# Performance work log

Measured on AMD Instinct MI355X. Metric: run time of the kernel, lower is better.

Reference implementation:

```python
import jax, jax.numpy as jnp
import numpy as np

N_NODES = 50000
N_EDGES = 800000
F_IN = 128
F_OUT = 128
EPS_STD = 1e-5  # PyG StdAggregation epsilon


def setup_inputs() -> dict:
    key = jax.random.key(0)
    ks = jax.random.split(key, 8)
    x = jax.random.normal(ks[0], (N_NODES, F_IN), dtype=jnp.float32)
    edge_index = jax.random.randint(ks[1], (2, N_EDGES), 0, N_NODES, dtype=jnp.int64)
    s = 0.02
    # pre_nn: Linear(2*F_IN -> F_IN)
    W_pre = jax.random.normal(ks[2], (2 * F_IN, F_IN), dtype=jnp.float32) * s
    b_pre = jnp.zeros((F_IN,), dtype=jnp.float32)
    # post_nn: Linear((1 + 4 aggregators * 1 scaler) * F_IN -> F_OUT)
    W_post = jax.random.normal(ks[3], (5 * F_IN, F_OUT), dtype=jnp.float32) * s
    b_post = jnp.zeros((F_OUT,), dtype=jnp.float32)
    # final lin: Linear(F_OUT -> F_OUT)
    W_lin = jax.random.normal(ks[4], (F_OUT, F_OUT), dtype=jnp.float32) * s
    b_lin = jnp.zeros((F_OUT,), dtype=jnp.float32)
    return {"x": x, "W_pre": W_pre, "b_pre": b_pre, "W_post": W_post,
            "b_post": b_post, "W_lin": W_lin, "b_lin": b_lin,
            "edge_index": edge_index}


def _pna_forward(x, W_pre, b_pre, W_post, b_post, W_lin, b_lin, edge_index):
    N = x.shape[0]
    src = edge_index[0]  # x_j (source / neighbor)
    dst = edge_index[1]  # x_i (target / aggregation index)

    # per-edge message: Linear(cat(x_i, x_j))  [E, F_IN]
    h = jnp.concatenate([x[dst], x[src]], axis=-1) @ W_pre + b_pre

    ones = jnp.ones((h.shape[0],), dtype=h.dtype)
    deg = jax.ops.segment_sum(ones, dst, num_segments=N)          # in-degree [N]
    deg_c = jnp.maximum(deg, 1.0)[:, None]

    s1 = jax.ops.segment_sum(h, dst, num_segments=N)
    s2 = jax.ops.segment_sum(h * h, dst, num_segments=N)
    mean = s1 / deg_c
    var = jax.nn.relu(s2 / deg_c - mean * mean)
    std = jnp.sqrt(var + EPS_STD)

    has_nb = (deg > 0)[:, None]
    mx = jax.ops.segment_max(h, dst, num_segments=N)
    mn = jax.ops.segment_min(h, dst, num_segments=N)
    mx = jnp.where(has_nb, mx, 0.0)
    mn = jnp.where(has_nb, mn, 0.0)

    # aggregators in declared order: mean, max, min, std -> [N, 4*F_IN]
    agg = jnp.concatenate([mean, mx, mn, std], axis=-1)

    # 'linear' degree scaler: deg / avg_deg
    avg_deg = jnp.mean(deg)
    agg = agg * (deg[:, None] / avg_deg)

    out = jnp.concatenate([x, agg], axis=-1) @ W_post + b_post
    out = out @ W_lin + b_lin
    return jax.nn.relu(out)


def reference(x, W_pre, b_pre, W_post, b_post, W_lin, b_lin, edge_index):
    return _pna_forward(x, W_pre, b_pre, W_post, b_post, W_lin, b_lin, edge_index)
```

## Files before the change

### kernel.cpp

```cpp
#include <hip/hip_runtime.h>
#include <hip/hip_bf16.h>
#include <math.h>


typedef _Float16 f16;
typedef _Float16 f16x8 __attribute__((ext_vector_type(8)));
typedef _Float16 f16x2 __attribute__((ext_vector_type(2)));
typedef float    f32x4 __attribute__((ext_vector_type(4)));

__device__ __forceinline__ unsigned packh2(float a, float b) {
  union { unsigned u; f16x2 h; } x; x.h = (f16x2){(f16)a, (f16)b}; return x.u;
}
__device__ __forceinline__ float2 unpackh2(unsigned v) {
  union { unsigned u; f16x2 h; } x; x.u = v;
  return make_float2((float)x.h.x, (float)x.h.y);
}

template<int KTOT, int KO1, bool HASB, bool RELU, bool OUTF16>
__global__ __launch_bounds__(256) void gemm_reg_k(
    const f16* __restrict__ A1, const f16* __restrict__ A2,
    const f16* __restrict__ Wt, const float* __restrict__ bias,
    float* __restrict__ outF, f16* __restrict__ outH, int M, int ldOut)
{
  const int tid = threadIdx.x;
  const int l   = tid & 63;
  const int w   = tid >> 6;
  const int wr  = (w >> 1) * 32;
  const int wc  = (w & 1) * 64;
  const int li  = l & 15, kg = l >> 4;
  const int rowBase = blockIdx.x * 64;
  const int colBase = blockIdx.y * 128;
  constexpr int ld2 = (KTOT > KO1) ? (KTOT - KO1) : 1;

  int aOff[2], a2Off[2], bOff[4];
#pragma unroll
  for (int r = 0; r < 2; ++r) {
    int gr = rowBase + wr + r * 16 + li; if (gr > M - 1) gr = M - 1;
    aOff[r] = gr * KO1; a2Off[r] = gr * ld2;
  }
#pragma unroll
  for (int c = 0; c < 4; ++c) bOff[c] = (colBase + wc + c * 16 + li) * KTOT;

  f32x4 acc[2][4];
#pragma unroll
  for (int r = 0; r < 2; ++r)
#pragma unroll
    for (int c = 0; c < 4; ++c) acc[r][c] = (f32x4){0.f, 0.f, 0.f, 0.f};

  f16x8 aA[2], bA[4], aB[2], bB[4];
  auto lf = [&](int k0, f16x8 a[2], f16x8 b[4]) {
    int k = k0 + kg * 8;
    if (KO1 == KTOT || k0 < KO1) {
#pragma unroll
      for (int r = 0; r < 2; ++r) a[r] = *reinterpret_cast<const f16x8*>(A1 + aOff[r] + k);
    } else {
#pragma unroll
      for (int r = 0; r < 2; ++r) a[r] = *reinterpret_cast<const f16x8*>(A2 + a2Off[r] + (k - KO1));
    }
#pragma unroll
    for (int c = 0; c < 4; ++c) b[c] = *reinterpret_cast<const f16x8*>(Wt + bOff[c] + k);
  };

  lf(0, aA, bA);
  for (int k0 = 0; k0 < KTOT; k0 += 64) {
    lf(k0 + 32, aB, bB);
#pragma unroll
    for (int r = 0; r < 2; ++r)
#pragma unroll
      for (int c = 0; c < 4; ++c)
        acc[r][c] = __builtin_amdgcn_mfma_f32_16x16x32_f16(aA[r], bA[c], acc[r][c], 0, 0, 0);
    if (k0 + 64 < KTOT) lf(k0 + 64, aA, bA);
#pragma unroll
    for (int r = 0; r < 2; ++r)
#pragma unroll
      for (int c = 0; c < 4; ++c)
        acc[r][c] = __builtin_amdgcn_mfma_f32_16x16x32_f16(aB[r], bB[c], acc[r][c], 0, 0, 0);
  }

  float bv[4];
#pragma unroll
  for (int c = 0; c < 4; ++c) {
    int col = colBase + wc + c * 16 + li;
    bv[c] = (HASB && col < 128) ? bias[col] : 0.f;
  }

  if constexpr (OUTF16) {
    __shared__ __align__(16) f16 Ls[64][136];
#pragma unroll
    for (int c = 0; c < 4; ++c) {
      int col = wc + c * 16 + li;
#pragma unroll
      for (int r = 0; r < 2; ++r)
#pragma unroll
        for (int j = 0; j < 4; ++j) {
          float v = acc[r][c][j] + bv[c];
          if (RELU) v = fmaxf(v, 0.f);
          Ls[wr + r * 16 + kg * 4 + j][col] = (f16)v;
        }
    }
    __syncthreads();
#pragma unroll
    for (int i = 0; i < 4; ++i) {
      int s = tid + 256 * i;
      int rr = s >> 4, cc = (s & 15) * 8;
      int gr = rowBase + rr;
      if (gr < M)
        *reinterpret_cast<float4*>(&outH[(size_t)gr * ldOut + colBase + cc]) =
            *reinterpret_cast<const float4*>(&Ls[rr][cc]);
    }
  } else {
    __shared__ __align__(16) float Lf[64][132];
#pragma unroll
    for (int c = 0; c < 4; ++c) {
      int col = wc + c * 16 + li;
#pragma unroll
      for (int r = 0; r < 2; ++r)
#pragma unroll
        for (int j = 0; j < 4; ++j) {
          float v = acc[r][c][j] + bv[c];
          if (RELU) v = fmaxf(v, 0.f);
          Lf[wr + r * 16 + kg * 4 + j][col] = v;
        }
    }
    __syncthreads();
#pragma unroll
    for (int i = 0; i < 8; ++i) {
      int s = tid + 256 * i;
      int rr = s >> 5, cc = (s & 31) * 4;
      int gr = rowBase + rr;
      if (gr < M)
        *reinterpret_cast<float4*>(&outF[(size_t)gr * ldOut + colBase + cc]) =
            *reinterpret_cast<const float4*>(&Lf[rr][cc]);
    }
  }
}

__global__ void cvt_x_k(const float* __restrict__ x, f16* __restrict__ xf, int n) {
  int i = (blockIdx.x * 256 + threadIdx.x) * 4;
  if (i < n) {
    float4 v = *reinterpret_cast<const float4*>(&x[i]);
    xf[i] = (f16)v.x; xf[i + 1] = (f16)v.y; xf[i + 2] = (f16)v.z; xf[i + 3] = (f16)v.w;
  }
}

__global__ void prep_wpre_k(const float* __restrict__ W, f16* __restrict__ Wt) {
  int e = blockIdx.x * 256 + threadIdx.x;
  if (e < 256 * 128) {
    int n = e >> 7, k = e & 127;
    float v = (n < 128) ? W[(size_t)k * 128 + n] : W[(size_t)(128 + k) * 128 + (n - 128)];
    Wt[e] = (f16)v;
  }
}

__global__ void fold_w_k(const float* __restrict__ Wpost, const float* __restrict__ bpost,
                         const float* __restrict__ Wlin,  const float* __restrict__ blin,
                         f16* __restrict__ WtComb, float* __restrict__ bcomb) {
  int e = blockIdx.x * 256 + threadIdx.x;
  if (e < 640 * 128) {
    int n = e / 640, k = e - n * 640;
    float s = 0.f;
#pragma unroll 4
    for (int m = 0; m < 128; ++m) s += Wpost[(size_t)k * 128 + m] * Wlin[(size_t)m * 128 + n];
    WtComb[(size_t)n * 640 + k] = (f16)s;
  } else if (e < 640 * 128 + 128) {
    int n = e - 640 * 128;
    float s = blin[n];
#pragma unroll 4
    for (int m = 0; m < 128; ++m) s += bpost[m] * Wlin[(size_t)m * 128 + n];
    bcomb[n] = s;
  }
}

__global__ void zero_k(int* __restrict__ p, int n) {
  int i = blockIdx.x * 256 + threadIdx.x;
  if (i < n) p[i] = 0;
}

__global__ void count_k(const int* __restrict__ ei, int* __restrict__ deg, int E) {
  int e = blockIdx.x * 256 + threadIdx.x;
  if (e < E) atomicAdd(&deg[ei[E + e]], 1);
}

__device__ __forceinline__ int blockExclScan(int v, int* wtot) {
  int lane = threadIdx.x & 63, wid = threadIdx.x >> 6;
  int x = v;
#pragma unroll
  for (int d = 1; d < 64; d <<= 1) {
    int y = __shfl_up(x, d);
    if (lane >= d) x += y;
  }
  if (lane == 63) wtot[wid] = x;
  __syncthreads();
  if (threadIdx.x == 0) {
    int s = 0;
#pragma unroll
    for (int k = 0; k < 4; ++k) { int t = wtot[k]; wtot[k] = s; s += t; }
  }
  __syncthreads();
  return wtot[wid] + x - v;
}

__global__ __launch_bounds__(256) void scan1_k(const int* __restrict__ deg,
                                               int* __restrict__ offs,
                                               int* __restrict__ partials, int n) {
  __shared__ int wtot[4];
  int i = blockIdx.x * 256 + threadIdx.x;
  int v = (i < n) ? deg[i] : 0;
  int e = blockExclScan(v, wtot);
  if (i < n) offs[i] = e;
  if (threadIdx.x == 255) partials[blockIdx.x] = e + v;
}

__global__ __launch_bounds__(256) void scan2_k(int* __restrict__ partials, int nb) {
  __shared__ int wtot[4];
  int v = (threadIdx.x < nb) ? partials[threadIdx.x] : 0;
  int e = blockExclScan(v, wtot);
  if (threadIdx.x < nb) partials[threadIdx.x] = e;
}

__global__ void scan3_k(const int* __restrict__ partials, int* __restrict__ offs,
                        int* __restrict__ cur, int n, int E) {
  int i = blockIdx.x * 256 + threadIdx.x;
  if (i < n) {
    int v = offs[i] + partials[i >> 8];
    offs[i] = v; cur[i] = v;
  }
  if (i == 0) offs[n] = E;
}

__global__ void scatter_k(const int* __restrict__ ei, int* __restrict__ cursor,
                          int* __restrict__ ssrc, int E) {
  int e = blockIdx.x * 256 + threadIdx.x;
  if (e < E) {
    int d = ei[E + e];
    int pos = atomicAdd(&cursor[d], 1);
    ssrc[pos] = ei[e];
  }
}

__global__ __launch_bounds__(256) void agg_k(
    const f16* __restrict__ CP, const int* __restrict__ offs,
    const int* __restrict__ ssrc, f16* __restrict__ AGG, int N)
{
  int w = threadIdx.x >> 6;
  int t = threadIdx.x & 63;
  int i = blockIdx.x * 4 + w;
  if (i >= N) return;
  int start = offs[i], end = offs[i + 1];
  int deg = end - start;
  unsigned* AGGu = (unsigned*)AGG;
  size_t o = (size_t)i * 256 + t;
  if (deg == 0) {
    AGGu[o] = 0u; AGGu[o + 64] = 0u; AGGu[o + 128] = 0u; AGGu[o + 192] = 0u;
    return;
  }
  const unsigned* CPu = (const unsigned*)CP;
  float s0 = 0.f, s1 = 0.f, q0 = 0.f, q1 = 0.f;
  float mx0 = -INFINITY, mx1 = -INFINITY, mn0 = INFINITY, mn1 = INFINITY;

  auto accum = [&](unsigned u) {
    float2 v = unpackh2(u);
    s0 += v.x; s1 += v.y;
    q0 = fmaf(v.x, v.x, q0); q1 = fmaf(v.y, v.y, q1);
    mx0 = fmaxf(mx0, v.x); mx1 = fmaxf(mx1, v.y);
    mn0 = fminf(mn0, v.x); mn1 = fminf(mn1, v.y);
  };

  for (int base = start; base < end; base += 64) {
    int cnt = min(end - base, 64);
    int myoff = 0;
    if (base + t < end) myoff = ssrc[base + t] * 128 + 64;
    int j = 0;
    for (; j + 4 <= cnt; j += 4) {
      int o0 = __shfl(myoff, j);
      int o1 = __shfl(myoff, j + 1);
      int o2 = __shfl(myoff, j + 2);
      int o3 = __shfl(myoff, j + 3);
      unsigned u0 = CPu[o0 + t];
      unsigned u1 = CPu[o1 + t];
      unsigned u2 = CPu[o2 + t];
      unsigned u3 = CPu[o3 + t];
      accum(u0); accum(u1); accum(u2); accum(u3);
    }
    for (; j < cnt; ++j) {
      int o0 = __shfl(myoff, j);
      accum(CPu[o0 + t]);
    }
  }

  float2 c = unpackh2(CPu[(size_t)i * 128 + t]);
  float degf = (float)deg;
  float inv = 1.f / degf;
  float m10 = s0 * inv, m11 = s1 * inv;
  float var0 = fmaxf(q0 * inv - m10 * m10, 0.f);
  float var1 = fmaxf(q1 * inv - m11 * m11, 0.f);
  float sd0 = sqrtf(var0 + 1e-5f), sd1 = sqrtf(var1 + 1e-5f);
  float sc = degf * (1.0f / 16.0f);
  AGGu[o]       = packh2((c.x + m10) * sc, (c.y + m11) * sc);
  AGGu[o + 64]  = packh2((c.x + mx0) * sc, (c.y + mx1) * sc);
  AGGu[o + 128] = packh2((c.x + mn0) * sc, (c.y + mn1) * sc);
  AGGu[o + 192] = packh2(sd0 * sc, sd1 * sc);
}

extern "C" void kernel_launch(void* const* d_in, const int* in_sizes, int n_in,
                              void* d_out, int out_size, void* d_ws, size_t ws_size,
                              hipStream_t stream) {
  const float* x      = (const float*)d_in[0];
  const float* W_pre  = (const float*)d_in[1];
  const float* b_pre  = (const float*)d_in[2];
  const float* W_post = (const float*)d_in[3];
  const float* b_post = (const float*)d_in[4];
  const float* W_lin  = (const float*)d_in[5];
  const float* b_lin  = (const float*)d_in[6];
  const int*   ei     = (const int*)d_in[7];

  const int N = in_sizes[0] / 128;
  const int E = in_sizes[7] / 2;

  char* ws = (char*)d_ws;
  size_t off = 0;
  auto alloc = [&](size_t bytes) -> void* {
    void* p = ws + off; off += (bytes + 255) & ~(size_t)255; return p;
  };
  f16*   xf     = (f16*)  alloc((size_t)N * 128 * 2);
  f16*   CP     = (f16*)  alloc((size_t)N * 256 * 2);
  f16*   AGG    = (f16*)  alloc((size_t)N * 512 * 2);
  f16*   WtPre  = (f16*)  alloc(256 * 128 * 2);
  f16*   WtComb = (f16*)  alloc(128 * 640 * 2);
  float* bcomb  = (float*)alloc(128 * 4);
  int*   ssrc   = (int*)  alloc((size_t)E * 4);
  int*   deg    = (int*)  alloc((size_t)N * 4);
  int*   offs   = (int*)  alloc((size_t)(N + 1) * 4);
  int*   cur    = (int*)  alloc((size_t)N * 4);
  int*   parts  = (int*)  alloc(1024 * 4);

  const int gTile = (N + 63) / 64;
  const int gE    = (E + 255) / 256;
  const int gN    = (N + 255) / 256;

  cvt_x_k<<<(N * 128 / 4 + 255) / 256, 256, 0, stream>>>(x, xf, N * 128);
  prep_wpre_k<<<(256 * 128 + 255) / 256, 256, 0, stream>>>(W_pre, WtPre);
  fold_w_k<<<(640 * 128 + 128 + 255) / 256, 256, 0, stream>>>(W_post, b_post, W_lin, b_lin, WtComb, bcomb);

  zero_k<<<gN, 256, 0, stream>>>(deg, N);

  gemm_reg_k<128, 128, true, false, true><<<dim3(gTile, 2), 256, 0, stream>>>(
      xf, nullptr, WtPre, b_pre, nullptr, CP, N, 256);

  count_k<<<gE, 256, 0, stream>>>(ei, deg, E);
  scan1_k<<<gN, 256, 0, stream>>>(deg, offs, parts, N);
  scan2_k<<<1, 256, 0, stream>>>(parts, gN);
  scan3_k<<<gN, 256, 0, stream>>>(parts, offs, cur, N, E);
  scatter_k<<<gE, 256, 0, stream>>>(ei, cur, ssrc, E);

  agg_k<<<(N + 3) / 4, 256, 0, stream>>>(CP, offs, ssrc, AGG, N);

  gemm_reg_k<640, 128, true, true, false><<<dim3(gTile, 1), 256, 0, stream>>>(
      xf, AGG, WtComb, bcomb, (float*)d_out, nullptr, N, 128);
}
```

Measured before the change: 312.7 us.

## Deepen GEMM register prefetch to four stages and merge setup kernels

The register-tiled MFMA GEMM now keeps four k-slices of A/B fragments in flight instead of two, so global loads are issued further ahead of their use. It also adds a launch bound of two blocks per CU. The weight transpose, weight folding and degree zeroing are merged into one setup kernel to cut launch count. The deeper prefetch raises register pressure, which may conflict with the new occupancy hint and cause spills.

```diff
diff --git a/kernel.cpp b/kernel.cpp
--- a/kernel.cpp
+++ b/kernel.cpp
@@ -17,7 +17,7 @@
 }
 
 template<int KTOT, int KO1, bool HASB, bool RELU, bool OUTF16>
-__global__ __launch_bounds__(256) void gemm_reg_k(
+__global__ __launch_bounds__(256, 2) void gemm_reg_k(
     const f16* __restrict__ A1, const f16* __restrict__ A2,
     const f16* __restrict__ Wt, const float* __restrict__ bias,
     float* __restrict__ outF, f16* __restrict__ outH, int M, int ldOut)
@@ -47,7 +47,6 @@
 #pragma unroll
     for (int c = 0; c < 4; ++c) acc[r][c] = (f32x4){0.f, 0.f, 0.f, 0.f};
 
-  f16x8 aA[2], bA[4], aB[2], bB[4];
   auto lf = [&](int k0, f16x8 a[2], f16x8 b[4]) {
     int k = k0 + kg * 8;
     if (KO1 == KTOT || k0 < KO1) {
@@ -60,21 +59,22 @@
 #pragma unroll
     for (int c = 0; c < 4; ++c) b[c] = *reinterpret_cast<const f16x8*>(Wt + bOff[c] + k);
   };
-
-  lf(0, aA, bA);
-  for (int k0 = 0; k0 < KTOT; k0 += 64) {
-    lf(k0 + 32, aB, bB);
+  auto mm = [&](f16x8 a[2], f16x8 b[4]) {
 #pragma unroll
     for (int r = 0; r < 2; ++r)
 #pragma unroll
       for (int c = 0; c < 4; ++c)
-        acc[r][c] = __builtin_amdgcn_mfma_f32_16x16x32_f16(aA[r], bA[c], acc[r][c], 0, 0, 0);
-    if (k0 + 64 < KTOT) lf(k0 + 64, aA, bA);
-#pragma unroll
-    for (int r = 0; r < 2; ++r)
-#pragma unroll
-      for (int c = 0; c < 4; ++c)
-        acc[r][c] = __builtin_amdgcn_mfma_f32_16x16x32_f16(aB[r], bB[c], acc[r][c], 0, 0, 0);
+        acc[r][c] = __builtin_amdgcn_mfma_f32_16x16x32_f16(a[r], b[c], acc[r][c], 0, 0, 0);
+  };
+
+  constexpr int NSTEP = KTOT / 32;
+  f16x8 a0[2], b0[4], a1[2], b1[4], a2[2], b2[4], a3[2], b3[4];
+  lf(0, a0, b0); lf(32, a1, b1); lf(64, a2, b2); lf(96, a3, b3);
+  for (int t = 0; t < NSTEP; t += 4) {
+    mm(a0, b0); if (t + 4 < NSTEP) lf((t + 4) * 32, a0, b0);
+    mm(a1, b1); if (t + 5 < NSTEP) lf((t + 5) * 32, a1, b1);
+    mm(a2, b2); if (t + 6 < NSTEP) lf((t + 6) * 32, a2, b2);
+    mm(a3, b3); if (t + 7 < NSTEP) lf((t + 7) * 32, a3, b3);
   }
 
   float bv[4];
@@ -143,37 +143,33 @@
   }
 }
 
-__global__ void prep_wpre_k(const float* __restrict__ W, f16* __restrict__ Wt) {
+__global__ void setup_k(const float* __restrict__ Wpre,
+                        const float* __restrict__ Wpost, const float* __restrict__ bpost,
+                        const float* __restrict__ Wlin,  const float* __restrict__ blin,
+                        f16* __restrict__ WtPre, f16* __restrict__ WtComb,
+                        float* __restrict__ bcomb, int* __restrict__ deg, int N) {
   int e = blockIdx.x * 256 + threadIdx.x;
   if (e < 256 * 128) {
     int n = e >> 7, k = e & 127;
-    float v = (n < 128) ? W[(size_t)k * 128 + n] : W[(size_t)(128 + k) * 128 + (n - 128)];
-    Wt[e] = (f16)v;
-  }
-}
-
-__global__ void fold_w_k(const float* __restrict__ Wpost, const float* __restrict__ bpost,
-                         const float* __restrict__ Wlin,  const float* __restrict__ blin,
-                         f16* __restrict__ WtComb, float* __restrict__ bcomb) {
-  int e = blockIdx.x * 256 + threadIdx.x;
-  if (e < 640 * 128) {
-    int n = e / 640, k = e - n * 640;
+    float v = (n < 128) ? Wpre[(size_t)k * 128 + n] : Wpre[(size_t)(128 + k) * 128 + (n - 128)];
+    WtPre[e] = (f16)v;
+  } else if (e < 256 * 128 + 640 * 128) {
+    int e2 = e - 256 * 128;
+    int n = e2 / 640, k = e2 - n * 640;
     float s = 0.f;
 #pragma unroll 4
     for (int m = 0; m < 128; ++m) s += Wpost[(size_t)k * 128 + m] * Wlin[(size_t)m * 128 + n];
     WtComb[(size_t)n * 640 + k] = (f16)s;
-  } else if (e < 640 * 128 + 128) {
-    int n = e - 640 * 128;
+  } else if (e < 256 * 128 + 640 * 128 + 128) {
+    int n = e - (256 * 128 + 640 * 128);
     float s = blin[n];
 #pragma unroll 4
     for (int m = 0; m < 128; ++m) s += bpost[m] * Wlin[(size_t)m * 128 + n];
     bcomb[n] = s;
-  }
-}
-
-__global__ void zero_k(int* __restrict__ p, int n) {
-  int i = blockIdx.x * 256 + threadIdx.x;
-  if (i < n) p[i] = 0;
+  } else {
+    int e3 = e - (256 * 128 + 640 * 128 + 128);
+    if (e3 < N) deg[e3] = 0;
+  }
 }
 
 __global__ void count_k(const int* __restrict__ ei, int* __restrict__ deg, int E) {
@@ -337,12 +333,11 @@
   const int gTile = (N + 63) / 64;
   const int gE    = (E + 255) / 256;
   const int gN    = (N + 255) / 256;
+  const int setupElems = 256 * 128 + 640 * 128 + 128 + N;
 
   cvt_x_k<<<(N * 128 / 4 + 255) / 256, 256, 0, stream>>>(x, xf, N * 128);
-  prep_wpre_k<<<(256 * 128 + 255) / 256, 256, 0, stream>>>(W_pre, WtPre);
-  fold_w_k<<<(640 * 128 + 128 + 255) / 256, 256, 0, stream>>>(W_post, b_post, W_lin, b_lin, WtComb, bcomb);
-
-  zero_k<<<gN, 256, 0, stream>>>(deg, N);
+  setup_k<<<(setupElems + 255) / 256, 256, 0, stream>>>(W_pre, W_post, b_post, W_lin, b_lin,
+                                                        WtPre, WtComb, bcomb, deg, N);
 
   gemm_reg_k<128, 128, true, false, true><<<dim3(gTile, 2), 256, 0, stream>>>(
       xf, nullptr, WtPre, b_pre, nullptr, CP, N, 256);
```

New measurement: 306.1 us. -2.1%, faster.
